# Kernel tuning notes

Measured on AMD Instinct MI355X. Metric: run time of the kernel, lower is better.

## Reference

```python
import jax, jax.numpy as jnp
import numpy as np

B, S, D, H, DH, F, K = 16, 1024, 384, 2, 192, 1536, 9  # batch, seq, d_model, heads, d_head, filter, kernel
EPS = 1e-5


def setup_inputs() -> dict:
    key = jax.random.key(0)
    ks = jax.random.split(key, 20)
    p = lambda k, shape: jax.random.normal(k, shape, dtype=jnp.float32) * 0.02
    return {
        "x": jax.random.normal(ks[0], (B, S, D), dtype=jnp.float32),
        "mask": jax.random.randint(ks[1], (B, S, S), 0, 2).astype(bool),
        # per-head QKV projections stacked over heads: [H, D, DH], biases [H, DH]
        "Wq": p(ks[2], (H, D, DH)), "bq": p(ks[3], (H, DH)),
        "Wk": p(ks[4], (H, D, DH)), "bk": p(ks[5], (H, DH)),
        "Wv": p(ks[6], (H, D, DH)), "bv": p(ks[7], (H, DH)),
        "Wo": p(ks[8], (D, D)), "bo": p(ks[9], (D,)),
        # conv kernels in lax WIO layout: [K, in, out] (== torch [out,in,K] transposed)
        "Wc1": p(ks[10], (K, D, F)), "bc1": p(ks[11], (F,)),
        "Wc2": p(ks[12], (K, F, D)), "bc2": p(ks[13], (D,)),
        "g1": jnp.ones((D,), jnp.float32), "beta1": jnp.zeros((D,), jnp.float32),
        "g2": jnp.ones((D,), jnp.float32), "beta2": jnp.zeros((D,), jnp.float32),
    }


def _layernorm(x, g, b):
    m = jnp.mean(x, axis=-1, keepdims=True)
    v = jnp.var(x, axis=-1, keepdims=True)
    return (x - m) / jnp.sqrt(v + EPS) * g + b


def reference(x, mask, Wq, bq, Wk, bk, Wv, bv, Wo, bo, Wc1, bc1, Wc2, bc2, g1, beta1, g2, beta2):
    residual = x
    # multi-head attention (heads vectorized instead of python loop)
    Q = jnp.einsum('bsd,hde->bhse', x, Wq) + bq[None, :, None, :]
    Kt = jnp.einsum('bsd,hde->bhse', x, Wk) + bk[None, :, None, :]
    V = jnp.einsum('bsd,hde->bhse', x, Wv) + bv[None, :, None, :]
    # NOTE: original scales by sqrt(d_model), not sqrt(d_head) — kept faithful
    QK = jnp.einsum('bhse,bhte->bhst', Q, Kt) / np.sqrt(D).astype(np.float32)
    QK = jnp.where(mask[:, None, :, :], jnp.float32(-1e9), QK)  # QK[mask] = -1e9
    A = jax.nn.softmax(QK, axis=-1)
    O = jnp.einsum('bhst,bhte->bhse', A, V)
    O = O.transpose(0, 2, 1, 3).reshape(O.shape[0], O.shape[2], H * DH)  # concat heads
    attn = O @ Wo + bo
    x = _layernorm(attn + residual, g1, beta1)  # dropout=0 (eval) is identity
    residual = x
    # conv1d FFN, padding='same'
    h = jax.lax.conv_general_dilated(x, Wc1, (1,), 'SAME', dimension_numbers=('NWC', 'WIO', 'NWC')) + bc1
    h = jax.nn.relu(h)
    h = jax.lax.conv_general_dilated(h, Wc2, (1,), 'SAME', dimension_numbers=('NWC', 'WIO', 'NWC')) + bc2
    x = _layernorm(h + residual, g2, beta2)
    return x
```

## Files before the change

kernel.cpp:

```cpp
#include <hip/hip_runtime.h>
#include <hip/hip_bf16.h>
#include <stdint.h>
#include <math.h>

typedef __attribute__((ext_vector_type(8))) short bf16x8;
typedef __attribute__((ext_vector_type(4))) float f32x4;
typedef __attribute__((ext_vector_type(4))) unsigned short u16x4;

#define DEV static __device__ __forceinline__

DEV unsigned short f2bf(float f){
  union { float f; unsigned u; } v; v.f = f;
  unsigned r = v.u + 0x7fffu + ((v.u >> 16) & 1u);
  return (unsigned short)(r >> 16);
}

DEV void gload_lds16(const void* g, void* l){
  __builtin_amdgcn_global_load_lds(
      (const __attribute__((address_space(1))) unsigned int*)g,
      (__attribute__((address_space(3))) unsigned int*)l, 16, 0, 0);
}


__global__ __launch_bounds__(256) void k_misc(const unsigned char* __restrict__ mb,
                                              unsigned* __restrict__ flag,
                                              unsigned short* __restrict__ zp){
  __shared__ unsigned s;
  if(threadIdx.x==0) s = 0;
  __syncthreads();
  unsigned any = 0;
  for(int off = threadIdx.x; off < 4096; off += 256) if(off & 3) any |= mb[off];
  if(any) atomicOr(&s, 1u);
  __syncthreads();
  if(threadIdx.x==0) *flag = (s ? 1u : 0u);
  for(int i = threadIdx.x; i < 2048; i += 256) zp[i] = 0;
}

__global__ __launch_bounds__(256) void k_cast4(const float* __restrict__ x,
                                               unsigned short* __restrict__ o, int n4){
  for(int i = blockIdx.x*256 + threadIdx.x; i < n4; i += gridDim.x*256){
    f32x4 v = ((const f32x4*)x)[i];
    u16x4 r;
    #pragma unroll
    for(int j=0;j<4;++j) r[j] = f2bf(v[j]);
    ((u16x4*)o)[i] = r;
  }
}

__global__ __launch_bounds__(256) void k_prep_qkv(const float* __restrict__ Wq, const float* __restrict__ Wk,
                                                  const float* __restrict__ Wv, const float* __restrict__ bq,
                                                  const float* __restrict__ bk, const float* __restrict__ bv,
                                                  unsigned short* __restrict__ Wt, float* __restrict__ bias){
  const int total = 1152*384;
  for(int idx = blockIdx.x*blockDim.x + threadIdx.x; idx < total; idx += gridDim.x*blockDim.x){
    int n = idx/384, d = idx%384;
    int mat = n/384, rem = n%384, h = rem/192, e = rem%192;
    const float* W = (mat==0) ? Wq : ((mat==1) ? Wk : Wv);
    Wt[idx] = f2bf(W[((size_t)h*384 + d)*192 + e]);
    if(d==0){
      const float* bb = (mat==0) ? bq : ((mat==1) ? bk : bv);
      bias[n] = bb[h*192 + e];
    }
  }
}

__global__ __launch_bounds__(256) void k_tr(const float* __restrict__ src,
                                            unsigned short* __restrict__ dst, int R, int C){
  __shared__ float t[32][33];
  const int tx = threadIdx.x & 31, ty = threadIdx.x >> 5;
  const int c0 = blockIdx.x*32, r0 = blockIdx.y*32;
  #pragma unroll
  for(int i=0;i<32;i+=8) t[ty+i][tx] = src[(size_t)(r0+ty+i)*C + c0+tx];
  __syncthreads();
  #pragma unroll
  for(int i=0;i<32;i+=8) dst[(size_t)(c0+ty+i)*R + r0+tx] = f2bf(t[tx][ty+i]);
}


template<int CIN, int NOUT>
__global__ __launch_bounds__(256)
void k_prepB(const float* __restrict__ W, unsigned short* __restrict__ Bf){
  constexpr int DTOT = CIN/64;
  const int gid = blockIdx.x*256 + threadIdx.x;
  const int lane = gid & 63;
  const int frag = gid >> 6;
  int f = frag;
  const int kk2 = f & 1, fn = (f>>1) & 3; f >>= 3;
  const int d = f % DTOT; f /= DTOT;
  const int t = f % 9;
  const int nq = f / 9;
  const int lane16 = lane & 15, laneh = lane >> 4;
  const int n = nq*64 + fn*16 + lane16;
  const int kbase = t*CIN + d*64 + kk2*32 + laneh*8;
  bf16x8 out;
  #pragma unroll
  for(int j=0;j<8;++j)
    out[j] = (short)f2bf(W[(size_t)(kbase + j)*NOUT + n]);
  *(bf16x8*)(Bf + (size_t)frag*512 + lane*8) = out;
}


template<int EPI>
__global__ __launch_bounds__(256)
void k_gemm(const unsigned short* __restrict__ A,
            const unsigned short* __restrict__ Bt,
            const float* __restrict__ bias,
            unsigned short* __restrict__ out_q,
            unsigned short* __restrict__ out_k,
            unsigned short* __restrict__ out_v,
            float* __restrict__ out_f,
            int Ktot, int lda)
{
  constexpr int BK = 64;
  __shared__ __attribute__((aligned(16))) unsigned short As[128*64];
  __shared__ __attribute__((aligned(16))) unsigned short Bs[128*64];
  const int tid = threadIdx.x;
  const int wave = tid >> 6, lane = tid & 63;
  const int lane16 = lane & 15, laneh = lane >> 4;
  const int wm = wave >> 1, wn = wave & 1;

  const int nwg  = gridDim.x*gridDim.y;
  const int flat = blockIdx.y*gridDim.x + blockIdx.x;
  const int swz  = (flat & 7)*(nwg >> 3) + (flat >> 3);
  const int m0 = (swz % gridDim.y) * 128;
  const int n0 = (swz / gridDim.y) * 128;

  f32x4 acc[4][4];
  #pragma unroll
  for(int i=0;i<4;++i)
    #pragma unroll
    for(int j=0;j<4;++j) acc[i][j] = (f32x4){0.f,0.f,0.f,0.f};

  const int nsteps = Ktot / BK;
  for(int ks=0; ks<nsteps; ++ks){
    const int kg = ks*BK;
    __syncthreads();
    #pragma unroll
    for(int q=0;q<4;++q){
      int e0 = (q*256 + tid)*8;
      int row = e0 >> 6, col = e0 & 63;
      gload_lds16(A + (size_t)(m0+row)*lda + kg + col, (char*)As + q*4096 + wave*1024);
    }
    #pragma unroll
    for(int q=0;q<4;++q){
      int e0 = (q*256 + tid)*8;
      int row = e0 >> 6, col = e0 & 63;
      gload_lds16(Bt + (size_t)(n0+row)*Ktot + kg + col, (char*)Bs + q*4096 + wave*1024);
    }
    __syncthreads();
    #pragma unroll
    for(int kk=0; kk<BK; kk+=32){
      bf16x8 af[4], bfr[4];
      #pragma unroll
      for(int fm=0;fm<4;++fm)
        af[fm] = *(const bf16x8*)&As[(wm*64 + fm*16 + lane16)*64 + kk + laneh*8];
      #pragma unroll
      for(int fn=0;fn<4;++fn)
        bfr[fn] = *(const bf16x8*)&Bs[(wn*64 + fn*16 + lane16)*64 + kk + laneh*8];
      #pragma unroll
      for(int fm=0;fm<4;++fm)
        #pragma unroll
        for(int fn=0;fn<4;++fn)
          acc[fm][fn] = __builtin_amdgcn_mfma_f32_16x16x32_bf16(af[fm], bfr[fn], acc[fm][fn], 0, 0, 0);
    }
  }
  #pragma unroll
  for(int fm=0;fm<4;++fm){
    #pragma unroll
    for(int fn=0;fn<4;++fn){
      #pragma unroll
      for(int r=0;r<4;++r){
        int gr = m0 + wm*64 + fm*16 + laneh*4 + r;
        int gc = n0 + wn*64 + fn*16 + lane16;
        float c = acc[fm][fn][r] + bias[gc];
        if(EPI==0){
          int mat = gc/384, rem = gc%384, h = rem/192, e = rem%192;
          int b = gr >> 10, s = gr & 1023;
          int bh = b*2 + h;
          if(mat==0)      out_q[((size_t)bh*1024 + s)*192 + e] = f2bf(c);
          else if(mat==1) out_k[((size_t)bh*1024 + s)*192 + e] = f2bf(c);
          else            out_v[((size_t)bh*192 + e)*1024 + s] = f2bf(c);
        } else {
          out_f[(size_t)gr*384 + gc] = c;
        }
      }
    }
  }
}


DEV void ldB8(bf16x8 (&r)[8], const unsigned short* __restrict__ Bf,
              int nq, int t, int DTOT, int dblk, int lane){
  const unsigned short* fb = Bf + ((size_t)((nq*9 + t)*DTOT) + dblk)*4096 + lane*8;
  #pragma unroll
  for(int f=0; f<8; ++f) r[f] = *(const bf16x8*)(fb + f*512);
}

template<int EPI, int CIN, int NOUT>
__global__ __launch_bounds__(256)
void k_conv(const unsigned short* __restrict__ A,
            const unsigned short* __restrict__ Bf,
            const float* __restrict__ bias,
            unsigned short* __restrict__ out_h,
            float* __restrict__ out_f,
            float* __restrict__ out_f2,
            const unsigned short* __restrict__ zp)
{
  __shared__ __attribute__((aligned(16))) unsigned short Ah[160*64];
  const int tid = threadIdx.x;
  const int wave = tid >> 6, lane = tid & 63;
  const int lane16 = lane & 15, laneh = lane >> 4;
  const int wm = wave >> 1, wn = wave & 1;

  const int nwg  = gridDim.x*gridDim.y;
  const int flat = blockIdx.y*gridDim.x + blockIdx.x;
  const int swz  = (flat & 7)*(nwg >> 3) + (flat >> 3);
  const int m0 = (swz % gridDim.y) * 128;
  const int n0 = (swz / gridDim.y) * 128;

  constexpr int DTOT = CIN/64;
  const int dper = DTOT / gridDim.z;
  const int dlo  = blockIdx.z * dper;
  const int srow = m0 & 1023;
  const int nq   = (n0 >> 6) + wn;

  f32x4 acc[4][4];
  #pragma unroll
  for(int i=0;i<4;++i)
    #pragma unroll
    for(int j=0;j<4;++j) acc[i][j] = (f32x4){0.f,0.f,0.f,0.f};

  bf16x8 b0[8], b1[8];

  for(int db=0; db<dper; ++db){
    const int dblk = dlo + db;
    if(db) __syncthreads();
    #pragma unroll
    for(int q=0;q<5;++q){
      int P = (q*256 + tid)*16;
      int row = P >> 7, cb = P & 127;
      int cs  = (cb ^ ((row&7)<<4)) >> 1;
      int s = srow - 4 + row;
      const unsigned short* src = (s >= 0 && s < 1024)
          ? A + (size_t)(m0 - 4 + row)*CIN + dblk*64 + cs : zp;
      gload_lds16(src, (char*)Ah + q*4096 + wave*1024);
    }
    ldB8(b0, Bf, nq, 0, DTOT, dblk, lane);
    __syncthreads();
    #pragma unroll
    for(int t=0; t<9; ++t){
      bf16x8 (&cur)[8] = (t & 1) ? b1 : b0;
      bf16x8 (&nxt)[8] = (t & 1) ? b0 : b1;
      if(t < 8) ldB8(nxt, Bf, nq, t+1, DTOT, dblk, lane);
      #pragma unroll
      for(int kk2=0; kk2<2; ++kk2){
        #pragma unroll
        for(int fm=0; fm<4; ++fm){
          int ra = wm*64 + fm*16 + lane16 + t;
          bf16x8 af = *(const bf16x8*)((const char*)Ah +
              ra*128 + (((kk2*32 + laneh*8)*2) ^ ((ra&7)<<4)));
          #pragma unroll
          for(int fn=0; fn<4; ++fn)
            acc[fm][fn] = __builtin_amdgcn_mfma_f32_16x16x32_bf16(af, cur[fn*2+kk2], acc[fm][fn], 0, 0, 0);
        }
      }
    }
  }
  float* out_p = (EPI==3 && blockIdx.z==2) ? out_f2
               : out_f + (size_t)blockIdx.z * 16384 * 384;
  #pragma unroll
  for(int fm=0;fm<4;++fm){
    #pragma unroll
    for(int fn=0;fn<4;++fn){
      #pragma unroll
      for(int r=0;r<4;++r){
        int gr = m0 + wm*64 + fm*16 + laneh*4 + r;
        int gc = n0 + wn*64 + fn*16 + lane16;
        float c = acc[fm][fn][r];
        if(EPI==2){
          c += bias[gc];
          out_h[(size_t)gr*NOUT + gc] = f2bf(fmaxf(c, 0.f));
        } else {
          out_p[(size_t)gr*384 + gc] = c;
        }
      }
    }
  }
}

__global__ __launch_bounds__(256)
void k_bias(const float* __restrict__ p, const float* __restrict__ bias,
            float* __restrict__ out, int n4){
  for(int i = blockIdx.x*256 + threadIdx.x; i < n4; i += gridDim.x*256){
    f32x4 a = ((const f32x4*)p)[i];
    f32x4 bi = ((const f32x4*)bias)[i % 96];
    ((f32x4*)out)[i] = a + bi;
  }
}


__global__ __launch_bounds__(256)
void k_attn(const unsigned short* __restrict__ Q,
            const unsigned short* __restrict__ Kb,
            const unsigned short* __restrict__ Vt,
            const void* __restrict__ mask,
            const unsigned* __restrict__ flag,
            unsigned short* __restrict__ O)
{
  __shared__ __attribute__((aligned(16))) unsigned short Ks[64*192];
  __shared__ __attribute__((aligned(16))) unsigned short Vs[192*64];
  __shared__ __attribute__((aligned(16))) unsigned short P_lds[4*16*64];

  const int flat = blockIdx.y*gridDim.x + blockIdx.x;
  const int w = (flat & 7)*64 + (flat >> 3);
  const int bh = w >> 4, qb = w & 15;
  const int b = bh >> 1, h = bh & 1;
  const int tid = threadIdx.x;
  const int wave = tid >> 6, lane = tid & 63;
  const int lane16 = lane & 15, laneh = lane >> 4;
  const int q0 = qb*64 + wave*16;
  const bool mbyte = (*flag != 0);
  const unsigned char* m8 = (const unsigned char*)mask;
  const int* m32 = (const int*)mask;
  unsigned short* Pw = P_lds + wave*1024;

  bf16x8 qa[6];
  {
    const unsigned short* Qrow = Q + ((size_t)bh*1024 + q0 + lane16)*192 + laneh*8;
    #pragma unroll
    for(int kk=0; kk<6; ++kk) qa[kk] = *(const bf16x8*)(Qrow + kk*32);
  }

  f32x4 accO[12];
  #pragma unroll
  for(int i=0;i<12;++i) accO[i] = (f32x4){0.f,0.f,0.f,0.f};
  float mrow[4], lrow[4];
  #pragma unroll
  for(int r=0;r<4;++r){ mrow[r] = -1e30f; lrow[r] = 0.f; }

  const float rs = 0.05103103630798288f;
  const size_t mbase = (size_t)b * 1024 * 1024;
  const unsigned short* Kbh = Kb + (size_t)bh*1024*192;
  const unsigned short* Vbh = Vt + (size_t)bh*192*1024;

  for(int t0=0; t0<1024; t0+=64){
    unsigned mskv[4][4];
    #pragma unroll
    for(int tf=0; tf<4; ++tf){
      #pragma unroll
      for(int r=0;r<4;++r){
        size_t mi = mbase + (size_t)(q0 + laneh*4 + r)*1024 + t0 + tf*16 + lane16;
        mskv[tf][r] = mbyte ? (unsigned)m8[mi] : (unsigned)m32[mi];
      }
    }
    __syncthreads();
    #pragma unroll
    for(int q=0;q<6;++q){
      int P = (q*256 + tid)*16;
      int row = P/384, cb = P%384;
      gload_lds16(Kbh + (size_t)(t0 + row)*192 + ((cb ^ ((row&7)<<4)) >> 1),
                  (char*)Ks + q*4096 + wave*1024);
    }
    #pragma unroll
    for(int q=0;q<6;++q){
      int P = (q*256 + tid)*16;
      int row = P >> 7, cb = P & 127;
      gload_lds16(Vbh + (size_t)row*1024 + t0 + ((cb ^ ((row&7)<<4)) >> 1),
                  (char*)Vs + q*4096 + wave*1024);
    }
    __syncthreads();
    f32x4 sc[4];
    #pragma unroll
    for(int i=0;i<4;++i) sc[i] = (f32x4){0.f,0.f,0.f,0.f};
    #pragma unroll
    for(int kk=0; kk<6; ++kk){
      #pragma unroll
      for(int tf=0; tf<4; ++tf){
        int tt = tf*16 + lane16;
        const bf16x8* kp = (const bf16x8*)((const char*)Ks +
            tt*384 + ((kk*64 + laneh*16) ^ ((tt&7)<<4)));
        sc[tf] = __builtin_amdgcn_mfma_f32_16x16x32_bf16(qa[kk], *kp, sc[tf], 0, 0, 0);
      }
    }
    #pragma unroll
    for(int tf=0; tf<4; ++tf)
      #pragma unroll
      for(int r=0;r<4;++r)
        sc[tf][r] = mskv[tf][r] ? -1e9f : sc[tf][r]*rs;
    float tm[4];
    #pragma unroll
    for(int r=0;r<4;++r){
      float v = fmaxf(fmaxf(sc[0][r],sc[1][r]), fmaxf(sc[2][r],sc[3][r]));
      v = fmaxf(v, __shfl_xor(v,1)); v = fmaxf(v, __shfl_xor(v,2));
      v = fmaxf(v, __shfl_xor(v,4)); v = fmaxf(v, __shfl_xor(v,8));
      tm[r] = v;
    }
    float scale_o[4];
    #pragma unroll
    for(int r=0;r<4;++r){
      float mn = fmaxf(mrow[r], tm[r]);
      scale_o[r] = __expf(mrow[r] - mn);
      mrow[r] = mn;
    }
    float ts[4] = {0.f,0.f,0.f,0.f};
    #pragma unroll
    for(int tf=0; tf<4; ++tf){
      #pragma unroll
      for(int r=0;r<4;++r){
        float p = __expf(sc[tf][r] - mrow[r]);
        ts[r] += p;
        Pw[(laneh*4 + r)*64 + tf*16 + lane16] = f2bf(p);
      }
    }
    #pragma unroll
    for(int r=0;r<4;++r){
      float v = ts[r];
      v += __shfl_xor(v,1); v += __shfl_xor(v,2); v += __shfl_xor(v,4); v += __shfl_xor(v,8);
      lrow[r] = lrow[r]*scale_o[r] + v;
    }
    #pragma unroll
    for(int ef=0; ef<12; ++ef)
      #pragma unroll
      for(int r=0;r<4;++r) accO[ef][r] *= scale_o[r];
    #pragma unroll
    for(int kk=0; kk<64; kk+=32){
      bf16x8 pa = *(const bf16x8*)&Pw[lane16*64 + kk + laneh*8];
      #pragma unroll
      for(int ef=0; ef<12; ++ef){
        int er = ef*16 + lane16;
        const bf16x8* vp = (const bf16x8*)((const char*)Vs +
            er*128 + (((kk + laneh*8)*2) ^ ((er&7)<<4)));
        accO[ef] = __builtin_amdgcn_mfma_f32_16x16x32_bf16(pa, *vp, accO[ef], 0, 0, 0);
      }
    }
  }
  #pragma unroll
  for(int ef=0; ef<12; ++ef){
    #pragma unroll
    for(int r=0;r<4;++r){
      int qr = q0 + laneh*4 + r;
      int e  = ef*16 + lane16;
      float o = accO[ef][r] / lrow[r];
      O[((size_t)b*1024 + qr)*384 + h*192 + e] = f2bf(o);
    }
  }
}


__global__ __launch_bounds__(256)
void k_ln(const float* __restrict__ a, const float* __restrict__ resid,
          const float* __restrict__ g, const float* __restrict__ beta,
          float* __restrict__ outf, unsigned short* __restrict__ outbf)
{
  const int row = blockIdx.x*4 + (threadIdx.x >> 6);
  const int lane = threadIdx.x & 63;
  const float* pa = a + (size_t)row*384;
  const float* pr = resid + (size_t)row*384;
  float v[6], s = 0.f, s2 = 0.f;
  #pragma unroll
  for(int j=0;j<6;++j){
    int e = lane + j*64;
    float t = pa[e] + pr[e];
    v[j] = t; s += t; s2 += t*t;
  }
  #pragma unroll
  for(int o=1;o<64;o<<=1){ s += __shfl_xor(s,o); s2 += __shfl_xor(s2,o); }
  float mean = s * (1.f/384.f);
  float var  = s2 * (1.f/384.f) - mean*mean;
  float inv  = rsqrtf(var + 1e-5f);
  #pragma unroll
  for(int j=0;j<6;++j){
    int e = lane + j*64;
    float t = (v[j]-mean)*inv*g[e] + beta[e];
    if(outf)  outf[(size_t)row*384 + e] = t;
    if(outbf) outbf[(size_t)row*384 + e] = f2bf(t);
  }
}

__global__ __launch_bounds__(256)
void k_lnred3(const float* __restrict__ p0, const float* __restrict__ p2,
              const float* __restrict__ bias, const float* __restrict__ resid,
              const float* __restrict__ g, const float* __restrict__ beta,
              float* __restrict__ outf)
{
  const int row = blockIdx.x*4 + (threadIdx.x >> 6);
  const int lane = threadIdx.x & 63;
  const float* p1 = p0 + (size_t)16384*384;
  const size_t base = (size_t)row*384;
  float v[6], s = 0.f, s2 = 0.f;
  #pragma unroll
  for(int j=0;j<6;++j){
    int e = lane + j*64;
    float t = p0[base+e] + p1[base+e] + p2[base+e] + bias[e] + resid[base+e];
    v[j] = t; s += t; s2 += t*t;
  }
  #pragma unroll
  for(int o=1;o<64;o<<=1){ s += __shfl_xor(s,o); s2 += __shfl_xor(s2,o); }
  float mean = s * (1.f/384.f);
  float var  = s2 * (1.f/384.f) - mean*mean;
  float inv  = rsqrtf(var + 1e-5f);
  #pragma unroll
  for(int j=0;j<6;++j){
    int e = lane + j*64;
    outf[base + e] = (v[j]-mean)*inv*g[e] + beta[e];
  }
}


extern "C" void kernel_launch(void* const* d_in, const int* in_sizes, int n_in,
                              void* d_out, int out_size, void* d_ws, size_t ws_size,
                              hipStream_t stream)
{
  const float* x   = (const float*)d_in[0];
  const void*  mask= d_in[1];
  const float* Wq  = (const float*)d_in[2];
  const float* bq  = (const float*)d_in[3];
  const float* Wk  = (const float*)d_in[4];
  const float* bk  = (const float*)d_in[5];
  const float* Wv  = (const float*)d_in[6];
  const float* bv  = (const float*)d_in[7];
  const float* Wo  = (const float*)d_in[8];
  const float* bo  = (const float*)d_in[9];
  const float* Wc1 = (const float*)d_in[10];
  const float* bc1 = (const float*)d_in[11];
  const float* Wc2 = (const float*)d_in[12];
  const float* bc2 = (const float*)d_in[13];
  const float* g1  = (const float*)d_in[14];
  const float* be1 = (const float*)d_in[15];
  const float* g2  = (const float*)d_in[16];
  const float* be2 = (const float*)d_in[17];

  char* ws = (char*)d_ws;
  size_t off = 0;
  auto alloc = [&](size_t bytes)->char*{
    char* p = ws + off; off += (bytes + 255) & ~(size_t)255; return p;
  };
  unsigned short* zp   = (unsigned short*)alloc(4096);
  unsigned*       flag = (unsigned*)alloc(256);
  unsigned short* wqkv = (unsigned short*)alloc((size_t)1152*384*2);
  float*          bqkv = (float*)alloc((size_t)1152*4);
  unsigned short* wot  = (unsigned short*)alloc((size_t)384*384*2);
  unsigned short* wc1t = (unsigned short*)alloc((size_t)1536*3456*2);
  unsigned short* wc2t = (unsigned short*)alloc((size_t)384*13824*2);
  unsigned short* xbf  = (unsigned short*)alloc((size_t)16384*384*2);
  unsigned short* Qb   = (unsigned short*)alloc((size_t)32*1024*192*2);
  unsigned short* Kbuf = (unsigned short*)alloc((size_t)32*1024*192*2);
  unsigned short* Vt   = (unsigned short*)alloc((size_t)32*192*1024*2);
  float*          yb   = (float*)alloc((size_t)16384*384*4);
  unsigned short* hb   = (unsigned short*)alloc((size_t)16384*1536*2);
  unsigned short* Obf  = xbf;
  unsigned short* x1bf = Qb;
  float*          x1f  = (float*)Kbuf;
  float*          zb   = yb;
  const size_t pb_bytes = (size_t)2*16384*384*4;
  const bool   splitk   = (ws_size >= off + pb_bytes);
  float*       pb       = (float*)alloc(pb_bytes);
  float*       slab2    = (float*)xbf;

  k_misc<<<1,256,0,stream>>>((const unsigned char*)mask, flag, zp);
  k_cast4<<<2048,256,0,stream>>>(x, xbf, 16384*384/4);
  k_prep_qkv<<<1728,256,0,stream>>>(Wq,Wk,Wv,bq,bk,bv,wqkv,bqkv);
  k_tr<<<dim3(12,12),256,0,stream>>>(Wo, wot, 384, 384);
  k_prepB<384,1536><<<2592,256,0,stream>>>(Wc1, wc1t);
  k_prepB<1536,384><<<2592,256,0,stream>>>(Wc2, wc2t);

  k_gemm<0><<<dim3(9,128),256,0,stream>>>(xbf, wqkv, bqkv, Qb, Kbuf, Vt,
                                          nullptr, 384, 384);
  k_attn<<<dim3(16,32),256,0,stream>>>(Qb, Kbuf, Vt, mask, flag, Obf);
  k_gemm<1><<<dim3(3,128),256,0,stream>>>(Obf, wot, bo, nullptr,nullptr,nullptr,
                                          yb, 384, 384);
  k_ln<<<4096,256,0,stream>>>(yb, x, g1, be1, x1f, x1bf);
  k_conv<2,384,1536><<<dim3(12,128,1),256,0,stream>>>(x1bf, wc1t, bc1, hb, nullptr, nullptr, zp);
  if(splitk){
    k_conv<3,1536,384><<<dim3(3,128,3),256,0,stream>>>(hb, wc2t, nullptr, nullptr, pb, slab2, zp);
    k_lnred3<<<4096,256,0,stream>>>(pb, slab2, bc2, x1f, g2, be2, (float*)d_out);
  } else {
    k_conv<3,1536,384><<<dim3(3,128,1),256,0,stream>>>(hb, wc2t, nullptr, nullptr, zb, nullptr, zp);
    k_bias<<<2048,256,0,stream>>>(zb, bc2, zb, 16384*384/4);
    k_ln<<<4096,256,0,stream>>>(zb, x1f, g2, be2, (float*)d_out, nullptr);
  }
}
```

Baseline: 536.7 us.

## Load conv A operand directly from global memory instead of LDS staging

The conv kernel no longer stages the shifted activation window into shared memory with barriers. Each wave now reads its A fragments straight from global memory per tap, relying on cache for the reuse across the nine taps, and runs one flattened tap loop with double-buffered B loads and raised wave priority around the MFMA block. This drops the LDS traffic and the per-block __syncthreads, but each A element is now fetched from global/L2 up to nine times and the loads are exposed in the MFMA loop without prefetch.

```diff
diff --git a/kernel.cpp b/kernel.cpp
--- a/kernel.cpp
+++ b/kernel.cpp
@@ -206,7 +206,6 @@
             float* __restrict__ out_f2,
             const unsigned short* __restrict__ zp)
 {
-  __shared__ __attribute__((aligned(16))) unsigned short Ah[160*64];
   const int tid = threadIdx.x;
   const int wave = tid >> 6, lane = tid & 63;
   const int lane16 = lane & 15, laneh = lane >> 4;
@@ -224,6 +223,9 @@
   const int srow = m0 & 1023;
   const int nq   = (n0 >> 6) + wn;
 
+  const int s0 = srow - 4 + wm*64 + lane16;
+  const unsigned short* Ab = A + ((size_t)(m0 - 4 + wm*64 + lane16))*CIN + laneh*8;
+
   f32x4 acc[4][4];
   #pragma unroll
   for(int i=0;i<4;++i)
@@ -231,41 +233,38 @@
     for(int j=0;j<4;++j) acc[i][j] = (f32x4){0.f,0.f,0.f,0.f};
 
   bf16x8 b0[8], b1[8];
-
-  for(int db=0; db<dper; ++db){
-    const int dblk = dlo + db;
-    if(db) __syncthreads();
-    #pragma unroll
-    for(int q=0;q<5;++q){
-      int P = (q*256 + tid)*16;
-      int row = P >> 7, cb = P & 127;
-      int cs  = (cb ^ ((row&7)<<4)) >> 1;
-      int s = srow - 4 + row;
-      const unsigned short* src = (s >= 0 && s < 1024)
-          ? A + (size_t)(m0 - 4 + row)*CIN + dblk*64 + cs : zp;
-      gload_lds16(src, (char*)Ah + q*4096 + wave*1024);
-    }
-    ldB8(b0, Bf, nq, 0, DTOT, dblk, lane);
-    __syncthreads();
-    #pragma unroll
-    for(int t=0; t<9; ++t){
-      bf16x8 (&cur)[8] = (t & 1) ? b1 : b0;
-      bf16x8 (&nxt)[8] = (t & 1) ? b0 : b1;
-      if(t < 8) ldB8(nxt, Bf, nq, t+1, DTOT, dblk, lane);
-      #pragma unroll
-      for(int kk2=0; kk2<2; ++kk2){
-        #pragma unroll
-        for(int fm=0; fm<4; ++fm){
-          int ra = wm*64 + fm*16 + lane16 + t;
-          bf16x8 af = *(const bf16x8*)((const char*)Ah +
-              ra*128 + (((kk2*32 + laneh*8)*2) ^ ((ra&7)<<4)));
-          #pragma unroll
-          for(int fn=0; fn<4; ++fn)
-            acc[fm][fn] = __builtin_amdgcn_mfma_f32_16x16x32_bf16(af, cur[fn*2+kk2], acc[fm][fn], 0, 0, 0);
-        }
-      }
-    }
-  }
+  ldB8(b0, Bf, nq, 0, DTOT, dlo, lane);
+
+  const int ntap = dper*9;
+  int tA = 0, dA = dlo;
+  int tP = 1, dP = dlo;
+
+  #define CONV_TAP(CUR)                                                        \
+    __builtin_amdgcn_s_setprio(1);                                             \
+    _Pragma("unroll")                                                          \
+    for(int kk2=0; kk2<2; ++kk2){                                              \
+      _Pragma("unroll")                                                        \
+      for(int fm=0; fm<4; ++fm){                                               \
+        int s = s0 + fm*16 + tA;                                               \
+        const unsigned short* ap = (s >= 0 && s < 1024)                        \
+            ? Ab + (size_t)(fm*16 + tA)*CIN + dA*64 + kk2*32 : zp;             \
+        bf16x8 af = *(const bf16x8*)ap;                                        \
+        _Pragma("unroll")                                                      \
+        for(int fn=0; fn<4; ++fn)                                              \
+          acc[fm][fn] = __builtin_amdgcn_mfma_f32_16x16x32_bf16(af, CUR[fn*2+kk2], acc[fm][fn], 0, 0, 0); \
+      }                                                                        \
+    }                                                                          \
+    __builtin_amdgcn_s_setprio(0);                                             \
+    if(++tA == 9){ tA = 0; ++dA; }
+
+  for(int i=0; i<ntap; i+=2){
+    if(i+1 < ntap){ ldB8(b1, Bf, nq, tP, DTOT, dP, lane); if(++tP==9){tP=0;++dP;} }
+    CONV_TAP(b0)
+    if(i+2 < ntap){ ldB8(b0, Bf, nq, tP, DTOT, dP, lane); if(++tP==9){tP=0;++dP;} }
+    CONV_TAP(b1)
+  }
+  #undef CONV_TAP
+
   float* out_p = (EPI==3 && blockIdx.z==2) ? out_f2
                : out_f + (size_t)blockIdx.z * 16384 * 384;
   #pragma unroll
```

New measurement: 1.089 ms, median of 3. 2.03x slower.
